# Kernel optimization log

Measured on AMD Instinct MI355X. Metric: run time of the kernel, lower is better.

The kernel has to match this reference:

```python
import jax, jax.numpy as jnp
import numpy as np

B, T, O = 8, 8, 25
C, H, W = 3, 192, 640
P = 16            # pooled output size / patch size
D = 768           # embed dim
GH, GW = 12, 2    # max adaptive sampling grid: ceil(H/P), ceil(2*r_max/P)


def setup_inputs() -> dict:
    key = jax.random.key(0)
    k1, k2, k3, k4, k5, k6 = jax.random.split(key, 6)
    features = jax.random.normal(k1, (B, C, T, H, W), jnp.float32)
    # keypoints (x, y, r); x >= H so that the source's buggy y2=min(x+r,H) still yields valid boxes
    kx = jax.random.uniform(k2, (B, T, O), minval=float(H), maxval=float(W))
    ky = jax.random.uniform(k3, (B, T, O), minval=0.0, maxval=float(H))
    kr = jax.random.uniform(k4, (B, T, O), minval=4.0, maxval=16.0)
    keypoints = jnp.stack([kx, ky, kr], axis=-1)
    conv_w = jax.random.normal(k5, (D, C, P, P), jnp.float32) * (1.0 / np.sqrt(C * P * P))
    conv_b = jax.random.normal(k6, (D,), jnp.float32) * 0.01
    return {"features": features, "keypoints": keypoints, "conv_w": conv_w, "conv_b": conv_b}


def _sample_coords(start, bin_sz, grid, G, size):
    # start,bin_sz,grid: [N]; returns coords y/x [N,P,G], validity mask, low idx, high idx, lerp weight
    N = start.shape[0]
    pb = jnp.arange(P, dtype=start.dtype)
    ig = jnp.arange(G, dtype=start.dtype)
    gf = jnp.maximum(grid, 1).astype(start.dtype)
    c = (start[:, None, None]
         + pb[None, :, None] * bin_sz[:, None, None]
         + (ig[None, None, :] + 0.5) * (bin_sz / gf)[:, None, None])  # [N,P,G]
    valid = (jnp.arange(G)[None, None, :] < grid[:, None, None]) & (c >= -1.0) & (c <= float(size))
    cc = jnp.clip(c, 0.0, float(size - 1))
    lo = jnp.floor(cc).astype(jnp.int32)
    hi = jnp.minimum(lo + 1, size - 1)
    l = cc - lo.astype(cc.dtype)  # fractional part (ly/lx)
    return valid, lo, hi, l


def _roi_align(feats_hw, boxes, img_idx):
    # feats_hw: [BT,H,W,C]; boxes: [N,4] xyxy; torchvision roi_align, aligned=True, sampling_ratio=-1
    x1, y1, x2, y2 = boxes[:, 0], boxes[:, 1], boxes[:, 2], boxes[:, 3]
    start_h, start_w = y1 - 0.5, x1 - 0.5  # aligned offset (spatial_scale=1)
    roi_h, roi_w = y2 - y1, x2 - x1        # aligned=True: no clamp to >=1
    bin_h, bin_w = roi_h / P, roi_w / P
    gh = jnp.ceil(roi_h / P).astype(jnp.int32)
    gw = jnp.ceil(roi_w / P).astype(jnp.int32)
    count = jnp.maximum(gh * gw, 1).astype(feats_hw.dtype)

    vy, y0, y1i, ly = _sample_coords(start_h, bin_h, gh, GH, H)  # [N,P,GH]
    vx, x0, x1i, lx = _sample_coords(start_w, bin_w, gw, GW, W)  # [N,P,GW]
    hy, hx = 1.0 - ly, 1.0 - lx

    def gather(yi, xi):  # -> [N,Ph,Pw,GH,GW,C]
        return feats_hw[img_idx[:, None, None, None, None],
                        yi[:, :, None, :, None],
                        xi[:, None, :, None, :]]

    w00 = hy[:, :, None, :, None] * hx[:, None, :, None, :]
    w01 = hy[:, :, None, :, None] * lx[:, None, :, None, :]
    w10 = ly[:, :, None, :, None] * hx[:, None, :, None, :]
    w11 = ly[:, :, None, :, None] * lx[:, None, :, None, :]
    val = (w00[..., None] * gather(y0, x0) + w01[..., None] * gather(y0, x1i)
           + w10[..., None] * gather(y1i, x0) + w11[..., None] * gather(y1i, x1i))
    mask = (vy[:, :, None, :, None] & vx[:, None, :, None, :])[..., None]
    val = jnp.where(mask, val, 0.0)
    return val.sum(axis=(3, 4)) / count[:, None, None, None]  # [N,P,P,C]


def _forward(features, keypoints, conv_w, conv_b):
    feats_hw = features.transpose(0, 2, 3, 4, 1).reshape(B * T, H, W, C)  # (b t) h w c
    kpts = keypoints.reshape(B * T * O, 3)
    kx, ky, kr = kpts[:, 0], kpts[:, 1], kpts[:, 2]
    # faithful to source (note: y2 uses x, a bug in the original module)
    bx1 = jnp.maximum(kx - kr, 0.0)
    by1 = jnp.maximum(ky - kr, 0.0)
    bx2 = jnp.minimum(kx + kr, float(W))
    by2 = jnp.minimum(kx + kr, float(H))
    boxes = jnp.stack([bx1, by1, bx2, by2], axis=-1)
    img_idx = jnp.arange(B * T * O, dtype=jnp.int32) // O
    pooled = _roi_align(feats_hw, boxes, img_idx)  # [N,P,P,C]
    # PxP conv with no padding on PxP input == flatten + linear
    out = jnp.einsum('nijc,dcij->nd', pooled, conv_w) + conv_b
    return out.reshape(B, T, O, D)


def reference(features, keypoints, conv_w, conv_b):
    return _forward(features, keypoints, conv_w, conv_b)
```

## Files before the change

kernel.cpp:

```cpp
#include <hip/hip_runtime.h>

#define NB 8
#define NT 8
#define NO 25
#define NC 3
#define NH 192
#define NW 640
#define NP 16
#define ND 768
#define NGH 12
#define NGW 2
#define NKP (NB*NT*NO)
#define NK (NC*NP*NP)
#define NTASK (NKP*NC)
#define NCVW ((NK*ND)/(256*4))

#define S_STRIDE 41

typedef __attribute__((ext_vector_type(4))) float  f32x4;
typedef __attribute__((ext_vector_type(8))) short  bf16x8;

static __device__ __forceinline__ unsigned short f2bf(float f) {
  union { float f; unsigned u; } x; x.f = f;
  unsigned r = x.u + 0x7FFFu + ((x.u >> 16) & 1u);
  return (unsigned short)(r >> 16);
}

__global__ __launch_bounds__(256) void pool_convw_kernel(
    const float* __restrict__ features,
    const float* __restrict__ keypoints,
    const float* __restrict__ conv_w,
    unsigned short* __restrict__ pooled,
    unsigned short* __restrict__ wbf)
{
  __shared__ float S[NH * S_STRIDE + 8];

  const int bid = blockIdx.x;
  const int tid = threadIdx.x;

  if (bid < NCVW) {
    const int i = bid * 256 + tid;
    const float4 v = reinterpret_cast<const float4*>(conv_w)[i];
    ushort4 o;
    o.x = f2bf(v.x); o.y = f2bf(v.y); o.z = f2bf(v.z); o.w = f2bf(v.w);
    reinterpret_cast<ushort4*>(wbf)[i] = o;
    return;
  }

  const int rb = bid - NCVW;
  const int t  = (rb & 7) * (NTASK / 8) + (rb >> 3);
  const int n  = t / 3;
  const int ch = t - 3 * n;

  const float kx = keypoints[n * 3 + 0];
  const float ky = keypoints[n * 3 + 1];
  const float kr = keypoints[n * 3 + 2];

  const float bx1 = fmaxf(kx - kr, 0.0f);
  const float by1 = fmaxf(ky - kr, 0.0f);
  const float bx2 = fminf(kx + kr, (float)NW);
  const float by2 = fminf(kx + kr, (float)NH);

  const float start_h = by1 - 0.5f;
  const float start_w = bx1 - 0.5f;
  const float bin_h = (by2 - by1) * (1.0f / (float)NP);
  const float bin_w = (bx2 - bx1) * (1.0f / (float)NP);
  const int gh = (int)ceilf(bin_h);
  const int gw = (int)ceilf(bin_w);
  const float ghf = (float)max(gh, 1);
  const float gwf = (float)max(gw, 1);
  const float inv_count = 1.0f / (float)max(gh * gw, 1);
  const float sub_h = bin_h / ghf;
  const float sub_w = bin_w / gwf;

  const float cy_min = start_h + 0.5f * sub_h;
  const float cy_max = start_h + 15.0f * bin_h + ((float)(gh - 1) + 0.5f) * sub_h;
  const float cx_min = start_w + 0.5f * sub_w;
  const float cx_max = start_w + 15.0f * bin_w + ((float)(gw - 1) + 0.5f) * sub_w;
  const int rmin = (int)floorf(fminf(fmaxf(cy_min, 0.0f), (float)(NH - 1)));
  const int rmax = min((int)floorf(fminf(fmaxf(cy_max, 0.0f), (float)(NH - 1))) + 1, NH - 1);
  const int cmin = (int)floorf(fminf(fmaxf(cx_min, 0.0f), (float)(NW - 1)));
  const int cmax = min((int)floorf(fminf(fmaxf(cx_max, 0.0f), (float)(NW - 1))) + 1, NW - 1);
  const int nrows = rmax - rmin + 1;
  const int cmin_al = cmin & ~3;
  const int nq = ((cmax - cmin_al) >> 2) + 1;
  const int tot = nrows * nq;
  const float inv_nq = 1.0f / (float)nq;

  const int img  = n / NO;
  const int bb   = img / NT;
  const int timg = img - bb * NT;
  const float* __restrict__ src =
      features + (size_t)((bb * NC + ch) * NT + timg) * (NH * NW);

  float4 v0, v1, v2, v3, v4, v5, v6, v7;
  int ro0, ro1, ro2, ro3, ro4, ro5, ro6, ro7;

#define STAGE_LOAD(Q, V, RO)                                                 \
  {                                                                          \
    const int e = tid + (Q << 8);                                            \
    if (e < tot) {                                                           \
      const int r  = (int)(((float)e + 0.5f) * inv_nq);                      \
      const int c4 = (e - r * nq) << 2;                                      \
      const int gc = cmin_al + c4;                                           \
      const float* p = src + (size_t)(rmin + r) * NW + gc;                   \
      if (gc + 3 < NW) { V = *reinterpret_cast<const float4*>(p); }          \
      else { V.x = p[0]; V.y = p[min(1, NW - 1 - gc)];                       \
             V.z = p[min(2, NW - 1 - gc)]; V.w = p[min(3, NW - 1 - gc)]; }   \
      RO = r * S_STRIDE + c4;                                                \
    } else { RO = -1; }                                                      \
  }

  STAGE_LOAD(0, v0, ro0) STAGE_LOAD(1, v1, ro1) STAGE_LOAD(2, v2, ro2)
  STAGE_LOAD(3, v3, ro3) STAGE_LOAD(4, v4, ro4) STAGE_LOAD(5, v5, ro5)
  STAGE_LOAD(6, v6, ro6) STAGE_LOAD(7, v7, ro7)
#undef STAGE_LOAD

#define STAGE_WRITE(V, RO)                                                   \
  if (RO >= 0) { float* s = &S[RO];                                          \
    s[0] = V.x; s[1] = V.y; s[2] = V.z; s[3] = V.w; }

  STAGE_WRITE(v0, ro0) STAGE_WRITE(v1, ro1) STAGE_WRITE(v2, ro2)
  STAGE_WRITE(v3, ro3) STAGE_WRITE(v4, ro4) STAGE_WRITE(v5, ro5)
  STAGE_WRITE(v6, ro6) STAGE_WRITE(v7, ro7)
#undef STAGE_WRITE

  if (tid < nrows) S[tid * S_STRIDE + (nq << 2)] = 0.0f;

  __syncthreads();

  const int i = tid >> 4;
  const int j = tid & 15;

  float hxv[NGW], lxv[NGW]; int cxv[NGW];
#pragma unroll
  for (int gx = 0; gx < NGW; ++gx) {
    const float c = start_w + (float)j * bin_w + ((float)gx + 0.5f) * sub_w;
    const float cc = fminf(fmaxf(c, 0.0f), (float)(NW - 1));
    const int x0 = (int)floorf(cc);
    const float lx = cc - (float)x0;
    const bool vx = gx < gw;
    lxv[gx] = vx ? lx : 0.0f;
    hxv[gx] = vx ? 1.0f - lx : 0.0f;
    cxv[gx] = min(x0 - cmin_al, nq << 2);
  }

  float acc = 0.0f;
#pragma unroll
  for (int gy = 0; gy < NGH; ++gy) {
    const float c = start_h + (float)i * bin_h + ((float)gy + 0.5f) * sub_h;
    const float cc = fminf(fmaxf(c, 0.0f), (float)(NH - 1));
    const int y0 = (int)floorf(cc);
    const float ly = cc - (float)y0;
    const bool vy = gy < gh;
    const float wl = vy ? ly : 0.0f;
    const float wh = vy ? 1.0f - ly : 0.0f;
    const int r0  = min(y0 - rmin, nrows - 1);
    const int ry0 = r0 * S_STRIDE;
    const int ry1 = min(r0 + 1, nrows - 1) * S_STRIDE;
#pragma unroll
    for (int gx = 0; gx < NGW; ++gx) {
      const float* p0 = &S[ry0 + cxv[gx]];
      const float* p1 = &S[ry1 + cxv[gx]];
      const float s00 = p0[0], s01 = p0[1];
      const float s10 = p1[0], s11 = p1[1];
      acc += wh * (hxv[gx] * s00 + lxv[gx] * s01)
           + wl * (hxv[gx] * s10 + lxv[gx] * s11);
    }
  }
  pooled[(size_t)n * NK + ch * (NP * NP) + tid] = f2bf(acc * inv_count);
}

#define BM 64
#define BN 64
#define BK 64

static __device__ __forceinline__ void gld_lds16(const unsigned short* g,
                                                 unsigned short* l) {
  __builtin_amdgcn_global_load_lds(
      (const __attribute__((address_space(1))) unsigned int*)g,
      (__attribute__((address_space(3))) unsigned int*)l,
      16, 0, 0);
}

__global__ __launch_bounds__(256) void gemm_kernel(
    const unsigned short* __restrict__ A,
    const unsigned short* __restrict__ Bw,
    const float* __restrict__ bias,
    float* __restrict__ outp)
{
  __shared__ __align__(16) unsigned short As[2][BM * BK];
  __shared__ __align__(16) unsigned short Bs[2][BM * BK];

  const int tid = threadIdx.x;
  const int w = tid >> 6;
  const int l = tid & 63;
  const int bm = blockIdx.x * BM;
  const int bn = blockIdx.y * BN;

  const int wr = w >> 1, wc = w & 1;
  const int lr = l & 15;
  const int kh = l >> 4;

  const int rA0 = (wr << 5) + lr;
  const int rB0 = (wc << 5) + lr;

#define STAGE(buf, kk)                                                       \
  {                                                                          \
    _Pragma("unroll")                                                        \
    for (int q = 0; q < 2; ++q) {                                            \
      const int s   = (q << 8) + tid;                                        \
      const int row = s >> 3;                                                \
      const int c16 = (s & 7) ^ (row & 7);                                   \
      gld_lds16(A  + (size_t)(bm + row) * NK + (kk) + (c16 << 3),            \
                &As[buf][s << 3]);                                           \
      gld_lds16(Bw + (size_t)(bn + row) * NK + (kk) + (c16 << 3),            \
                &Bs[buf][s << 3]);                                           \
    }                                                                        \
  }

  f32x4 acc[2][2] = {};

  STAGE(0, 0)
  __syncthreads();

  int cur = 0;
  for (int it = 0; it < NK / BK; ++it) {
    if (it + 1 < NK / BK) STAGE(cur ^ 1, (it + 1) * BK)

#pragma unroll
    for (int ks = 0; ks < 2; ++ks) {
      const int kq = (ks << 2) + kh;
      const bf16x8 a0 = *reinterpret_cast<const bf16x8*>(
          &As[cur][(rA0 << 6) + ((kq ^ (rA0 & 7)) << 3)]);
      const bf16x8 a1 = *reinterpret_cast<const bf16x8*>(
          &As[cur][((rA0 + 16) << 6) + ((kq ^ (rA0 & 7)) << 3)]);
      const bf16x8 b0 = *reinterpret_cast<const bf16x8*>(
          &Bs[cur][(rB0 << 6) + ((kq ^ (rB0 & 7)) << 3)]);
      const bf16x8 b1 = *reinterpret_cast<const bf16x8*>(
          &Bs[cur][((rB0 + 16) << 6) + ((kq ^ (rB0 & 7)) << 3)]);
      acc[0][0] = __builtin_amdgcn_mfma_f32_16x16x32_bf16(a0, b0, acc[0][0], 0, 0, 0);
      acc[0][1] = __builtin_amdgcn_mfma_f32_16x16x32_bf16(a0, b1, acc[0][1], 0, 0, 0);
      acc[1][0] = __builtin_amdgcn_mfma_f32_16x16x32_bf16(a1, b0, acc[1][0], 0, 0, 0);
      acc[1][1] = __builtin_amdgcn_mfma_f32_16x16x32_bf16(a1, b1, acc[1][1], 0, 0, 0);
    }

    __syncthreads();
    cur ^= 1;
  }
#undef STAGE

#pragma unroll
  for (int ni = 0; ni < 2; ++ni) {
    const int col = bn + (wc << 5) + (ni << 4) + lr;
    const float bv = bias[col];
#pragma unroll
    for (int mi = 0; mi < 2; ++mi) {
      const int rbase = bm + (wr << 5) + (mi << 4) + (kh << 2);
#pragma unroll
      for (int q = 0; q < 4; ++q) {
        outp[(size_t)(rbase + q) * ND + col] = acc[mi][ni][q] + bv;
      }
    }
  }
}

extern "C" void kernel_launch(void* const* d_in, const int* in_sizes, int n_in,
                              void* d_out, int out_size, void* d_ws, size_t ws_size,
                              hipStream_t stream) {
  (void)in_sizes; (void)n_in; (void)out_size; (void)ws_size;
  const float* features  = (const float*)d_in[0];
  const float* keypoints = (const float*)d_in[1];
  const float* conv_w    = (const float*)d_in[2];
  const float* conv_b    = (const float*)d_in[3];
  float* outp = (float*)d_out;

  unsigned short* pooled = (unsigned short*)d_ws;
  unsigned short* wbf    = (unsigned short*)((char*)d_ws + 2457600);

  pool_convw_kernel<<<NCVW + NTASK, 256, 0, stream>>>(features, keypoints,
                                                      conv_w, pooled, wbf);

  dim3 grid(NKP / BM, ND / BN);
  gemm_kernel<<<grid, 256, 0, stream>>>(pooled, wbf, conv_b, outp);
}
```

Measured before the change: 38.74 us.

## Split ROI pooling blocks by output-row halves and split sample rows across thread pairs

Each ROI/channel task is now handled by two blocks, one for each half of the 16 output rows. Each block stages only the input rows its half needs, so the LDS tile shrinks to 100 rows and the staging loads drop from 8 to 4 per thread. Within a block, each output element is computed by two lanes, each taking 6 of the 12 vertical sample rows, and the partial sums are combined with a shuffle. The goal is more blocks, higher occupancy and shorter per-thread sample loops, at the cost of reading keypoints and redoing coordinate setup twice per task, plus possibly re-staging some boundary rows.

```diff
diff --git a/kernel.cpp b/kernel.cpp
--- a/kernel.cpp
+++ b/kernel.cpp
@@ -13,9 +13,11 @@
 #define NKP (NB*NT*NO)
 #define NK (NC*NP*NP)
 #define NTASK (NKP*NC)
+#define NSPLIT (NTASK*2)
 #define NCVW ((NK*ND)/(256*4))
 
 #define S_STRIDE 41
+#define S_ROWS 100
 
 typedef __attribute__((ext_vector_type(4))) float  f32x4;
 typedef __attribute__((ext_vector_type(8))) short  bf16x8;
@@ -33,7 +35,7 @@
     unsigned short* __restrict__ pooled,
     unsigned short* __restrict__ wbf)
 {
-  __shared__ float S[NH * S_STRIDE + 8];
+  __shared__ float S[S_ROWS * S_STRIDE + 8];
 
   const int bid = blockIdx.x;
   const int tid = threadIdx.x;
@@ -47,10 +49,12 @@
     return;
   }
 
-  const int rb = bid - NCVW;
-  const int t  = (rb & 7) * (NTASK / 8) + (rb >> 3);
-  const int n  = t / 3;
-  const int ch = t - 3 * n;
+  const int rb      = bid - NCVW;
+  const int logical = (rb & 7) * (NSPLIT / 8) + (rb >> 3);
+  const int task    = logical >> 1;
+  const int half    = logical & 1;
+  const int n  = task / 3;
+  const int ch = task - 3 * n;
 
   const float kx = keypoints[n * 3 + 0];
   const float ky = keypoints[n * 3 + 1];
@@ -73,8 +77,10 @@
   const float sub_h = bin_h / ghf;
   const float sub_w = bin_w / gwf;
 
-  const float cy_min = start_h + 0.5f * sub_h;
-  const float cy_max = start_h + 15.0f * bin_h + ((float)(gh - 1) + 0.5f) * sub_h;
+  const int i_lo = half << 3;
+
+  const float cy_min = start_h + (float)i_lo * bin_h + 0.5f * sub_h;
+  const float cy_max = start_h + (float)(i_lo + 7) * bin_h + ((float)(gh - 1) + 0.5f) * sub_h;
   const float cx_min = start_w + 0.5f * sub_w;
   const float cx_max = start_w + 15.0f * bin_w + ((float)(gw - 1) + 0.5f) * sub_w;
   const int rmin = (int)floorf(fminf(fmaxf(cy_min, 0.0f), (float)(NH - 1)));
@@ -93,8 +99,8 @@
   const float* __restrict__ src =
       features + (size_t)((bb * NC + ch) * NT + timg) * (NH * NW);
 
-  float4 v0, v1, v2, v3, v4, v5, v6, v7;
-  int ro0, ro1, ro2, ro3, ro4, ro5, ro6, ro7;
+  float4 v0, v1, v2, v3;
+  int ro0, ro1, ro2, ro3;
 
 #define STAGE_LOAD(Q, V, RO)                                                 \
   {                                                                          \
@@ -111,26 +117,25 @@
     } else { RO = -1; }                                                      \
   }
 
-  STAGE_LOAD(0, v0, ro0) STAGE_LOAD(1, v1, ro1) STAGE_LOAD(2, v2, ro2)
-  STAGE_LOAD(3, v3, ro3) STAGE_LOAD(4, v4, ro4) STAGE_LOAD(5, v5, ro5)
-  STAGE_LOAD(6, v6, ro6) STAGE_LOAD(7, v7, ro7)
+  STAGE_LOAD(0, v0, ro0) STAGE_LOAD(1, v1, ro1)
+  STAGE_LOAD(2, v2, ro2) STAGE_LOAD(3, v3, ro3)
 #undef STAGE_LOAD
 
 #define STAGE_WRITE(V, RO)                                                   \
   if (RO >= 0) { float* s = &S[RO];                                          \
     s[0] = V.x; s[1] = V.y; s[2] = V.z; s[3] = V.w; }
 
-  STAGE_WRITE(v0, ro0) STAGE_WRITE(v1, ro1) STAGE_WRITE(v2, ro2)
-  STAGE_WRITE(v3, ro3) STAGE_WRITE(v4, ro4) STAGE_WRITE(v5, ro5)
-  STAGE_WRITE(v6, ro6) STAGE_WRITE(v7, ro7)
+  STAGE_WRITE(v0, ro0) STAGE_WRITE(v1, ro1)
+  STAGE_WRITE(v2, ro2) STAGE_WRITE(v3, ro3)
 #undef STAGE_WRITE
 
   if (tid < nrows) S[tid * S_STRIDE + (nq << 2)] = 0.0f;
 
   __syncthreads();
 
-  const int i = tid >> 4;
-  const int j = tid & 15;
+  const int i = i_lo + (tid >> 5);
+  const int j = (tid >> 1) & 15;
+  const int h = tid & 1;
 
   float hxv[NGW], lxv[NGW]; int cxv[NGW];
 #pragma unroll
@@ -147,7 +152,8 @@
 
   float acc = 0.0f;
 #pragma unroll
-  for (int gy = 0; gy < NGH; ++gy) {
+  for (int gg = 0; gg < 6; ++gg) {
+    const int gy = h * 6 + gg;
     const float c = start_h + (float)i * bin_h + ((float)gy + 0.5f) * sub_h;
     const float cc = fminf(fmaxf(c, 0.0f), (float)(NH - 1));
     const int y0 = (int)floorf(cc);
@@ -168,7 +174,9 @@
            + wl * (hxv[gx] * s10 + lxv[gx] * s11);
     }
   }
-  pooled[(size_t)n * NK + ch * (NP * NP) + tid] = f2bf(acc * inv_count);
+  acc += __shfl_xor(acc, 1);
+  if (h == 0)
+    pooled[(size_t)n * NK + ch * (NP * NP) + (i << 4) + j] = f2bf(acc * inv_count);
 }
 
 #define BM 64
@@ -278,8 +286,8 @@
   unsigned short* pooled = (unsigned short*)d_ws;
   unsigned short* wbf    = (unsigned short*)((char*)d_ws + 2457600);
 
-  pool_convw_kernel<<<NCVW + NTASK, 256, 0, stream>>>(features, keypoints,
-                                                      conv_w, pooled, wbf);
+  pool_convw_kernel<<<NCVW + NSPLIT, 256, 0, stream>>>(features, keypoints,
+                                                       conv_w, pooled, wbf);
 
   dim3 grid(NKP / BM, ND / BN);
   gemm_kernel<<<grid, 256, 0, stream>>>(pooled, wbf, conv_b, outp);
```

New measurement: 38.97 us. About the same (+0.6%).
